# Kernel optimization log

Measured on AMD Instinct MI355X. Metric: run time of the kernel, lower is better.

## Reference

```python
import jax, jax.numpy as jnp
import numpy as np

SCALE = 1.0 / np.sqrt(128.0).astype(np.float32)  # 1/sqrt(head_dim)


def setup_inputs() -> dict:
    key = jax.random.key(0)
    kq, kk, kv = jax.random.split(key, 3)
    B, S, D = 32, 2048, 128
    q = jax.random.normal(kq, (B, S, D), dtype=jnp.float32)
    k = jax.random.normal(kk, (B, S, D), dtype=jnp.float32)
    v = jax.random.normal(kv, (B, S, D), dtype=jnp.float32)
    return {"q": q, "k": k, "v": v}


def reference(q, k, v):
    # attention = bmm(q, k^T) * scale ; softmax over last (key) dim; bmm with v
    scores = jnp.einsum("bsd,btd->bst", q, k) * SCALE  # [B, S, S]
    attn = jax.nn.softmax(scores, axis=-1)
    return jnp.einsum("bst,btd->bsd", attn, v)  # [B, S, D]
```

## Files before the change

### kernel.cpp

```cpp
#include <hip/hip_runtime.h>
#include <math.h>
#include <stdint.h>

typedef __bf16 bf16_t;
typedef __bf16 bf16x2 __attribute__((ext_vector_type(2)));
typedef __bf16 bf16x4 __attribute__((ext_vector_type(4)));
typedef __bf16 bf16x8 __attribute__((ext_vector_type(8)));
typedef float f32x4 __attribute__((ext_vector_type(4)));

#define NB   32
#define SEQ  2048
#define HD   128
#define SCALE 0.08838834764831845f
#define LOG2E 1.4426950408889634f

__device__ __forceinline__ float fast_exp2(float x) {
#if __has_builtin(__builtin_amdgcn_exp2f)
  return __builtin_amdgcn_exp2f(x);
#else
  return exp2f(x);
#endif
}

__global__ __launch_bounds__(256) void prep_kernel(
    const float* __restrict__ K, const float* __restrict__ V,
    bf16_t* __restrict__ Kb, bf16_t* __restrict__ Vt)
{
  const int b = blockIdx.x;
  const int tid = threadIdx.x;
  if (b < 2048) {
    size_t base4 = (size_t)b * 1024;
#pragma unroll
    for (int i = 0; i < 4; ++i) {
      size_t idx = base4 + tid + i * 256;
      float4 x = ((const float4*)K)[idx];
      bf16x4 y;
      y[0] = (bf16_t)x.x; y[1] = (bf16_t)x.y;
      y[2] = (bf16_t)x.z; y[3] = (bf16_t)x.w;
      ((bf16x4*)Kb)[idx] = y;
    }
  } else {
    __shared__ float tile[64][65];
    const int bt = b - 2048;
    const int batch = bt >> 6;
    const int rem = bt & 63;
    const int s0 = (rem >> 1) * 64;
    const int d0 = (rem & 1) * 64;
#pragma unroll
    for (int i = 0; i < 4; ++i) {
      int e = tid + i * 256;
      int s = e >> 4, dq = e & 15;
      float4 x = *(const float4*)&V[((size_t)batch * SEQ + s0 + s) * HD + d0 + dq * 4];
      tile[s][dq * 4 + 0] = x.x;
      tile[s][dq * 4 + 1] = x.y;
      tile[s][dq * 4 + 2] = x.z;
      tile[s][dq * 4 + 3] = x.w;
    }
    __syncthreads();
#pragma unroll
    for (int i = 0; i < 2; ++i) {
      int g = tid + i * 256;
      int d = g >> 3, sg = g & 7;
      bf16x8 w;
#pragma unroll
      for (int j = 0; j < 8; ++j) w[j] = (bf16_t)tile[sg * 8 + j][d];
      *(bf16x8*)&Vt[((size_t)batch * HD + d0 + d) * SEQ + s0 + sg * 8] = w;
    }
  }
}

__global__ __launch_bounds__(256) void fa6_kernel(
    const float* __restrict__ Q, const bf16_t* __restrict__ Kbf,
    const bf16_t* __restrict__ Vt, float* __restrict__ O)
{
  __shared__ __attribute__((aligned(16))) bf16_t Ksw[2][64 * 128];
  __shared__ __attribute__((aligned(16))) bf16_t Vsw[2][128 * 64];
  __shared__ __attribute__((aligned(16))) bf16_t Psh[4][16][72];

  const int tid  = threadIdx.x;
  const int lane = tid & 63;
  const int wq   = tid >> 6;
  const int quad = lane >> 4;
  const int l15  = lane & 15;

  const int batch = blockIdx.x >> 5;
  const int qt    = blockIdx.x & 31;

  const float*  Qb = Q   + ((size_t)batch * SEQ + qt * 64) * HD;
  const bf16_t* Kb = Kbf + (size_t)batch * SEQ * HD;
  const bf16_t* Vb = Vt  + (size_t)batch * HD * SEQ;
  float*        Ob = O   + ((size_t)batch * SEQ + qt * 64) * HD;

  bf16x8 aq[4];
  {
    const int qrow = wq * 16 + l15;
    const float qs = SCALE * LOG2E;
#pragma unroll
    for (int kf = 0; kf < 4; ++kf) {
      const float* qp = Qb + (size_t)qrow * HD + kf * 32 + quad * 8;
      float4 x0 = *(const float4*)qp;
      float4 x1 = *(const float4*)(qp + 4);
      bf16x8 a;
      a[0] = (bf16_t)(x0.x * qs); a[1] = (bf16_t)(x0.y * qs);
      a[2] = (bf16_t)(x0.z * qs); a[3] = (bf16_t)(x0.w * qs);
      a[4] = (bf16_t)(x1.x * qs); a[5] = (bf16_t)(x1.y * qs);
      a[6] = (bf16_t)(x1.z * qs); a[7] = (bf16_t)(x1.w * qs);
      aq[kf] = a;
    }
  }

  f32x4 o[8];
#pragma unroll
  for (int t = 0; t < 8; ++t) { o[t][0]=0.f; o[t][1]=0.f; o[t][2]=0.f; o[t][3]=0.f; }
  float m_r = -INFINITY, l_r = 0.0f;

  auto stage = [&](int buf, int kb) {
#pragma unroll
    for (int i = 0; i < 4; ++i) {
      int row = wq * 16 + i * 4 + (lane >> 4);
      int gk = (lane & 15) ^ (row & 15);
      const bf16_t* gp = Kb + (size_t)(kb + row) * HD + gk * 8;
      __builtin_amdgcn_global_load_lds(
          (const __attribute__((address_space(1))) void*)gp,
          (__attribute__((address_space(3))) void*)&Ksw[buf][(wq * 16 + i * 4) * 128],
          16, 0, 0);
    }
#pragma unroll
    for (int i = 0; i < 4; ++i) {
      int d = wq * 32 + i * 8 + (lane >> 3);
      int gv = (lane & 7) ^ (d & 7);
      const bf16_t* gp = Vb + (size_t)d * SEQ + kb + gv * 8;
      __builtin_amdgcn_global_load_lds(
          (const __attribute__((address_space(1))) void*)gp,
          (__attribute__((address_space(3))) void*)&Vsw[buf][(wq * 32 + i * 8) * 64],
          16, 0, 0);
    }
  };

  stage(0, 0);

  for (int it = 0; it < SEQ / 64; ++it) {
    __syncthreads();
    if (it + 1 < SEQ / 64) stage((it + 1) & 1, (it + 1) * 64);

    const bf16_t* Ks = &Ksw[it & 1][0];
    const bf16_t* Vs = &Vsw[it & 1][0];

    f32x4 s[4];
#pragma unroll
    for (int ct = 0; ct < 4; ++ct) { s[ct][0]=0.f; s[ct][1]=0.f; s[ct][2]=0.f; s[ct][3]=0.f; }
    __builtin_amdgcn_s_setprio(1);
#pragma unroll
    for (int kf = 0; kf < 4; ++kf)
#pragma unroll
      for (int ct = 0; ct < 4; ++ct) {
        int row = ct * 16 + l15;
        bf16x8 ak = *(const bf16x8*)&Ks[row * 128 + (((kf * 4 + quad) ^ l15) * 8)];
        s[ct] = __builtin_amdgcn_mfma_f32_16x16x32_bf16(ak, aq[kf], s[ct], 0, 0, 0);
      }
    __builtin_amdgcn_s_setprio(0);

    float mx = s[0][0];
#pragma unroll
    for (int ct = 0; ct < 4; ++ct)
#pragma unroll
      for (int r = 0; r < 4; ++r) mx = fmaxf(mx, s[ct][r]);
    mx = fmaxf(mx, __shfl_xor(mx, 16));
    mx = fmaxf(mx, __shfl_xor(mx, 32));

    bf16x8 av0[8], av1[8];
#pragma unroll
    for (int t = 0; t < 8; ++t) {
      const int d = t * 16 + l15;
      av0[t] = *(const bf16x8*)&Vs[d * 64 + ((quad ^ (l15 & 7)) * 8)];
      av1[t] = *(const bf16x8*)&Vs[d * 64 + (((4 + quad) ^ (l15 & 7)) * 8)];
    }

    if (!__all(mx <= m_r + 8.0f)) {
      const float mnew = fmaxf(m_r, mx);
      const float alpha = fast_exp2(m_r - mnew);
      m_r = mnew;
      l_r *= alpha;
#pragma unroll
      for (int t = 0; t < 8; ++t) {
        o[t][0]*=alpha; o[t][1]*=alpha; o[t][2]*=alpha; o[t][3]*=alpha;
      }
    }

    float ls = 0.f;
#pragma unroll
    for (int ct = 0; ct < 4; ++ct)
#pragma unroll
      for (int r = 0; r < 4; ++r) {
        float p = fast_exp2(s[ct][r] - m_r);
        s[ct][r] = p; ls += p;
      }

#pragma unroll
    for (int ct = 0; ct < 4; ++ct) {
      bf16x4 pp;
      pp[0]=(bf16_t)s[ct][0]; pp[1]=(bf16_t)s[ct][1];
      pp[2]=(bf16_t)s[ct][2]; pp[3]=(bf16_t)s[ct][3];
      *(bf16x4*)&Psh[wq][l15][ct * 16 + quad * 4] = pp;
    }
    ls += __shfl_xor(ls, 16);
    ls += __shfl_xor(ls, 32);
    l_r += ls;
    asm volatile("s_waitcnt lgkmcnt(0)" ::: "memory");
    bf16x8 ap0 = *(const bf16x8*)&Psh[wq][l15][quad * 8];
    bf16x8 ap1 = *(const bf16x8*)&Psh[wq][l15][32 + quad * 8];

    __builtin_amdgcn_s_setprio(1);
#pragma unroll
    for (int t = 0; t < 8; ++t) {
      o[t] = __builtin_amdgcn_mfma_f32_16x16x32_bf16(av0[t], ap0, o[t], 0, 0, 0);
      o[t] = __builtin_amdgcn_mfma_f32_16x16x32_bf16(av1[t], ap1, o[t], 0, 0, 0);
    }
    __builtin_amdgcn_s_setprio(0);
  }

  float inv = 1.0f / l_r;
  const int qrow = wq * 16 + l15;
#pragma unroll
  for (int t = 0; t < 8; ++t) {
    float4 w;
    w.x = o[t][0]*inv; w.y = o[t][1]*inv; w.z = o[t][2]*inv; w.w = o[t][3]*inv;
    *(float4*)&Ob[(size_t)qrow * HD + t * 16 + quad * 4] = w;
  }
}

#define BM   64
#define BN   64
#define KPAD 8
#define VPAD 8
#define PPAD 8

__global__ __launch_bounds__(256) void fa_fallback(
    const float* __restrict__ Q, const float* __restrict__ K,
    const float* __restrict__ V, float* __restrict__ O)
{
  __shared__ __attribute__((aligned(16))) bf16_t Ksh[BN][HD + KPAD];
  __shared__ __attribute__((aligned(16))) bf16_t Vsh[HD][BN + VPAD];
  __shared__ __attribute__((aligned(16))) bf16_t Psh[4][16][BN + PPAD];

  const int tid = threadIdx.x;
  const int lane = tid & 63;
  const int wq = tid >> 6;
  const int quad = lane >> 4;
  const int l15 = lane & 15;
  const int bid = blockIdx.x;
  const int batch = bid >> 5;
  const int qt = bid & 31;

  const float* Qb = Q + (size_t)batch * SEQ * HD + (size_t)qt * BM * HD;
  const float* Kb = K + (size_t)batch * SEQ * HD;
  const float* Vb = V + (size_t)batch * SEQ * HD;
  float* Ob = O + (size_t)batch * SEQ * HD + (size_t)qt * BM * HD;

  bf16x8 aq[4];
  {
    const int qrow = wq * 16 + l15;
#pragma unroll
    for (int kf = 0; kf < 4; ++kf) {
      const float* qp = Qb + (size_t)qrow * HD + kf * 32 + quad * 8;
      float4 x0 = *(const float4*)(qp);
      float4 x1 = *(const float4*)(qp + 4);
      bf16x8 a;
      a[0] = (bf16_t)(x0.x * SCALE); a[1] = (bf16_t)(x0.y * SCALE);
      a[2] = (bf16_t)(x0.z * SCALE); a[3] = (bf16_t)(x0.w * SCALE);
      a[4] = (bf16_t)(x1.x * SCALE); a[5] = (bf16_t)(x1.y * SCALE);
      a[6] = (bf16_t)(x1.z * SCALE); a[7] = (bf16_t)(x1.w * SCALE);
      aq[kf] = a;
    }
  }

  f32x4 o[8];
#pragma unroll
  for (int t = 0; t < 8; ++t) { o[t][0]=0.f; o[t][1]=0.f; o[t][2]=0.f; o[t][3]=0.f; }
  float m_r = -INFINITY, l_r = 0.0f;
  const int vkp = (tid & 31) * 2;
  const int vg = tid >> 5;
  float4 kreg[8], vreg[8];

#pragma unroll
  for (int i = 0; i < 8; ++i) {
    int v = tid + i * 256, row = v >> 5, c4 = (v & 31) * 4;
    kreg[i] = *(const float4*)(Kb + (size_t)row * HD + c4);
  }
#pragma unroll
  for (int i = 0; i < 4; ++i) {
    int d0 = (vg + i * 8) * 4;
    const float* vp0 = Vb + (size_t)vkp * HD + d0;
    vreg[2 * i] = *(const float4*)vp0;
    vreg[2 * i + 1] = *(const float4*)(vp0 + HD);
  }

  for (int kb = 0; kb < SEQ; kb += BN) {
    __syncthreads();
#pragma unroll
    for (int i = 0; i < 8; ++i) {
      int v = tid + i * 256, row = v >> 5, c4 = (v & 31) * 4;
      float4 kv = kreg[i];
      bf16x4 kk;
      kk[0]=(bf16_t)kv.x; kk[1]=(bf16_t)kv.y; kk[2]=(bf16_t)kv.z; kk[3]=(bf16_t)kv.w;
      *(bf16x4*)&Ksh[row][c4] = kk;
    }
#pragma unroll
    for (int i = 0; i < 4; ++i) {
      int d0 = (vg + i * 8) * 4;
      float4 a0 = vreg[2 * i], a1 = vreg[2 * i + 1];
      bf16x2 p0; p0[0]=(bf16_t)a0.x; p0[1]=(bf16_t)a1.x;
      bf16x2 p1; p1[0]=(bf16_t)a0.y; p1[1]=(bf16_t)a1.y;
      bf16x2 p2; p2[0]=(bf16_t)a0.z; p2[1]=(bf16_t)a1.z;
      bf16x2 p3; p3[0]=(bf16_t)a0.w; p3[1]=(bf16_t)a1.w;
      *(bf16x2*)&Vsh[d0 + 0][vkp] = p0;
      *(bf16x2*)&Vsh[d0 + 1][vkp] = p1;
      *(bf16x2*)&Vsh[d0 + 2][vkp] = p2;
      *(bf16x2*)&Vsh[d0 + 3][vkp] = p3;
    }
    __syncthreads();

    const int kbn = kb + BN;
    if (kbn < SEQ) {
#pragma unroll
      for (int i = 0; i < 8; ++i) {
        int v = tid + i * 256, row = v >> 5, c4 = (v & 31) * 4;
        kreg[i] = *(const float4*)(Kb + (size_t)(kbn + row) * HD + c4);
      }
#pragma unroll
      for (int i = 0; i < 4; ++i) {
        int d0 = (vg + i * 8) * 4;
        const float* vp0 = Vb + (size_t)(kbn + vkp) * HD + d0;
        vreg[2 * i] = *(const float4*)vp0;
        vreg[2 * i + 1] = *(const float4*)(vp0 + HD);
      }
    }

    f32x4 s[4];
#pragma unroll
    for (int ct = 0; ct < 4; ++ct) { s[ct][0]=0.f; s[ct][1]=0.f; s[ct][2]=0.f; s[ct][3]=0.f; }
#pragma unroll
    for (int kf = 0; kf < 4; ++kf)
#pragma unroll
      for (int ct = 0; ct < 4; ++ct) {
        bf16x8 ak = *(const bf16x8*)&Ksh[ct * 16 + l15][kf * 32 + quad * 8];
        s[ct] = __builtin_amdgcn_mfma_f32_16x16x32_bf16(ak, aq[kf], s[ct], 0, 0, 0);
      }

    float mx = s[0][0];
#pragma unroll
    for (int ct = 0; ct < 4; ++ct)
#pragma unroll
      for (int r = 0; r < 4; ++r) mx = fmaxf(mx, s[ct][r]);
    mx = fmaxf(mx, __shfl_xor(mx, 16));
    mx = fmaxf(mx, __shfl_xor(mx, 32));
    float mnew = fmaxf(m_r, mx);
    float alpha = __expf(m_r - mnew);
    m_r = mnew;
    float ls = 0.f;
#pragma unroll
    for (int ct = 0; ct < 4; ++ct)
#pragma unroll
      for (int r = 0; r < 4; ++r) {
        float p = __expf(s[ct][r] - mnew);
        s[ct][r] = p; ls += p;
      }
    ls += __shfl_xor(ls, 16);
    ls += __shfl_xor(ls, 32);
    l_r = l_r * alpha + ls;

#pragma unroll
    for (int ct = 0; ct < 4; ++ct) {
      bf16x4 pp;
      pp[0]=(bf16_t)s[ct][0]; pp[1]=(bf16_t)s[ct][1];
      pp[2]=(bf16_t)s[ct][2]; pp[3]=(bf16_t)s[ct][3];
      *(bf16x4*)&Psh[wq][l15][ct * 16 + quad * 4] = pp;
    }
    asm volatile("s_waitcnt lgkmcnt(0)" ::: "memory");
    bf16x8 ap0 = *(const bf16x8*)&Psh[wq][l15][quad * 8];
    bf16x8 ap1 = *(const bf16x8*)&Psh[wq][l15][32 + quad * 8];

#pragma unroll
    for (int t = 0; t < 8; ++t) {
      o[t][0]*=alpha; o[t][1]*=alpha; o[t][2]*=alpha; o[t][3]*=alpha;
    }
#pragma unroll
    for (int t = 0; t < 8; ++t) {
      bf16x8 av0 = *(const bf16x8*)&Vsh[t * 16 + l15][quad * 8];
      o[t] = __builtin_amdgcn_mfma_f32_16x16x32_bf16(av0, ap0, o[t], 0, 0, 0);
      bf16x8 av1 = *(const bf16x8*)&Vsh[t * 16 + l15][32 + quad * 8];
      o[t] = __builtin_amdgcn_mfma_f32_16x16x32_bf16(av1, ap1, o[t], 0, 0, 0);
    }
  }

  float inv = 1.0f / l_r;
  const int qrow = wq * 16 + l15;
#pragma unroll
  for (int t = 0; t < 8; ++t) {
    float4 w;
    w.x = o[t][0]*inv; w.y = o[t][1]*inv; w.z = o[t][2]*inv; w.w = o[t][3]*inv;
    *(float4*)&Ob[(size_t)qrow * HD + t * 16 + quad * 4] = w;
  }
}

extern "C" void kernel_launch(void* const* d_in, const int* in_sizes, int n_in,
                              void* d_out, int out_size, void* d_ws, size_t ws_size,
                              hipStream_t stream) {
  const float* q = (const float*)d_in[0];
  const float* k = (const float*)d_in[1];
  const float* v = (const float*)d_in[2];
  float* out = (float*)d_out;

  const size_t elems = (size_t)NB * SEQ * HD;
  const size_t need = elems * 2 * 2;

  if (ws_size >= need) {
    bf16_t* Kb = (bf16_t*)d_ws;
    bf16_t* Vt = Kb + elems;
    prep_kernel<<<4096, 256, 0, stream>>>(k, v, Kb, Vt);
    fa6_kernel<<<NB * (SEQ / 64), 256, 0, stream>>>(q, Kb, Vt, out);
  } else {
    fa_fallback<<<NB * (SEQ / BM), 256, 0, stream>>>(q, k, v, out);
  }
}
```

Measured before the change: 246.7 us.

## Process two 64-row query groups per block to reuse K/V tiles

```diff
diff --git a/kernel.cpp b/kernel.cpp
--- a/kernel.cpp
+++ b/kernel.cpp
@@ -69,7 +69,7 @@
   }
 }
 
-__global__ __launch_bounds__(256) void fa6_kernel(
+__global__ __launch_bounds__(256) void fa7_kernel(
     const float* __restrict__ Q, const bf16_t* __restrict__ Kbf,
     const bf16_t* __restrict__ Vt, float* __restrict__ O)
 {
@@ -83,36 +83,43 @@
   const int quad = lane >> 4;
   const int l15  = lane & 15;
 
-  const int batch = blockIdx.x >> 5;
-  const int qt    = blockIdx.x & 31;
-
-  const float*  Qb = Q   + ((size_t)batch * SEQ + qt * 64) * HD;
+  const int L     = ((blockIdx.x & 7) << 6) | (blockIdx.x >> 3);
+  const int batch = L >> 4;
+  const int qt    = L & 15;
+
+  const float*  Qb = Q   + ((size_t)batch * SEQ + qt * 128) * HD;
   const bf16_t* Kb = Kbf + (size_t)batch * SEQ * HD;
   const bf16_t* Vb = Vt  + (size_t)batch * HD * SEQ;
-  float*        Ob = O   + ((size_t)batch * SEQ + qt * 64) * HD;
-
-  bf16x8 aq[4];
+  float*        Ob = O   + ((size_t)batch * SEQ + qt * 128) * HD;
+
+  bf16x8 aq[2][4];
   {
-    const int qrow = wq * 16 + l15;
     const float qs = SCALE * LOG2E;
 #pragma unroll
-    for (int kf = 0; kf < 4; ++kf) {
-      const float* qp = Qb + (size_t)qrow * HD + kf * 32 + quad * 8;
-      float4 x0 = *(const float4*)qp;
-      float4 x1 = *(const float4*)(qp + 4);
-      bf16x8 a;
-      a[0] = (bf16_t)(x0.x * qs); a[1] = (bf16_t)(x0.y * qs);
-      a[2] = (bf16_t)(x0.z * qs); a[3] = (bf16_t)(x0.w * qs);
-      a[4] = (bf16_t)(x1.x * qs); a[5] = (bf16_t)(x1.y * qs);
-      a[6] = (bf16_t)(x1.z * qs); a[7] = (bf16_t)(x1.w * qs);
-      aq[kf] = a;
-    }
-  }
-
-  f32x4 o[8];
-#pragma unroll
-  for (int t = 0; t < 8; ++t) { o[t][0]=0.f; o[t][1]=0.f; o[t][2]=0.f; o[t][3]=0.f; }
-  float m_r = -INFINITY, l_r = 0.0f;
+    for (int g = 0; g < 2; ++g) {
+      const int qrow = g * 64 + wq * 16 + l15;
+#pragma unroll
+      for (int kf = 0; kf < 4; ++kf) {
+        const float* qp = Qb + (size_t)qrow * HD + kf * 32 + quad * 8;
+        float4 x0 = *(const float4*)qp;
+        float4 x1 = *(const float4*)(qp + 4);
+        bf16x8 a;
+        a[0] = (bf16_t)(x0.x * qs); a[1] = (bf16_t)(x0.y * qs);
+        a[2] = (bf16_t)(x0.z * qs); a[3] = (bf16_t)(x0.w * qs);
+        a[4] = (bf16_t)(x1.x * qs); a[5] = (bf16_t)(x1.y * qs);
+        a[6] = (bf16_t)(x1.z * qs); a[7] = (bf16_t)(x1.w * qs);
+        aq[g][kf] = a;
+      }
+    }
+  }
+
+  f32x4 o[2][8];
+#pragma unroll
+  for (int g = 0; g < 2; ++g)
+#pragma unroll
+    for (int t = 0; t < 8; ++t) { o[g][t][0]=0.f; o[g][t][1]=0.f; o[g][t][2]=0.f; o[g][t][3]=0.f; }
+  float m_r0 = -INFINITY, l_r0 = 0.0f;
+  float m_r1 = -INFINITY, l_r1 = 0.0f;
 
   auto stage = [&](int buf, int kb) {
 #pragma unroll
@@ -146,27 +153,77 @@
     const bf16_t* Ks = &Ksw[it & 1][0];
     const bf16_t* Vs = &Vsw[it & 1][0];
 
-    f32x4 s[4];
-#pragma unroll
-    for (int ct = 0; ct < 4; ++ct) { s[ct][0]=0.f; s[ct][1]=0.f; s[ct][2]=0.f; s[ct][3]=0.f; }
-    __builtin_amdgcn_s_setprio(1);
+    f32x4 s[2][4];
+#pragma unroll
+    for (int g = 0; g < 2; ++g)
+#pragma unroll
+      for (int ct = 0; ct < 4; ++ct) { s[g][ct][0]=0.f; s[g][ct][1]=0.f; s[g][ct][2]=0.f; s[g][ct][3]=0.f; }
 #pragma unroll
     for (int kf = 0; kf < 4; ++kf)
 #pragma unroll
       for (int ct = 0; ct < 4; ++ct) {
         int row = ct * 16 + l15;
         bf16x8 ak = *(const bf16x8*)&Ks[row * 128 + (((kf * 4 + quad) ^ l15) * 8)];
-        s[ct] = __builtin_amdgcn_mfma_f32_16x16x32_bf16(ak, aq[kf], s[ct], 0, 0, 0);
-      }
-    __builtin_amdgcn_s_setprio(0);
-
-    float mx = s[0][0];
+        s[0][ct] = __builtin_amdgcn_mfma_f32_16x16x32_bf16(ak, aq[0][kf], s[0][ct], 0, 0, 0);
+        s[1][ct] = __builtin_amdgcn_mfma_f32_16x16x32_bf16(ak, aq[1][kf], s[1][ct], 0, 0, 0);
+      }
+
+    float mx0 = s[0][0][0], mx1 = s[1][0][0];
 #pragma unroll
     for (int ct = 0; ct < 4; ++ct)
 #pragma unroll
-      for (int r = 0; r < 4; ++r) mx = fmaxf(mx, s[ct][r]);
-    mx = fmaxf(mx, __shfl_xor(mx, 16));
-    mx = fmaxf(mx, __shfl_xor(mx, 32));
+      for (int r = 0; r < 4; ++r) {
+        mx0 = fmaxf(mx0, s[0][ct][r]);
+        mx1 = fmaxf(mx1, s[1][ct][r]);
+      }
+    mx0 = fmaxf(mx0, __shfl_xor(mx0, 16));
+    mx1 = fmaxf(mx1, __shfl_xor(mx1, 16));
+    mx0 = fmaxf(mx0, __shfl_xor(mx0, 32));
+    mx1 = fmaxf(mx1, __shfl_xor(mx1, 32));
+
+    if (!__all(mx0 <= m_r0 + 8.0f)) {
+      const float mnew = fmaxf(m_r0, mx0);
+      const float alpha = fast_exp2(m_r0 - mnew);
+      m_r0 = mnew; l_r0 *= alpha;
+#pragma unroll
+      for (int t = 0; t < 8; ++t) {
+        o[0][t][0]*=alpha; o[0][t][1]*=alpha; o[0][t][2]*=alpha; o[0][t][3]*=alpha;
+      }
+    }
+    if (!__all(mx1 <= m_r1 + 8.0f)) {
+      const float mnew = fmaxf(m_r1, mx1);
+      const float alpha = fast_exp2(m_r1 - mnew);
+      m_r1 = mnew; l_r1 *= alpha;
+#pragma unroll
+      for (int t = 0; t < 8; ++t) {
+        o[1][t][0]*=alpha; o[1][t][1]*=alpha; o[1][t][2]*=alpha; o[1][t][3]*=alpha;
+      }
+    }
+
+    float ls0 = 0.f, ls1 = 0.f;
+#pragma unroll
+    for (int ct = 0; ct < 4; ++ct)
+#pragma unroll
+      for (int r = 0; r < 4; ++r) {
+        float p0 = fast_exp2(s[0][ct][r] - m_r0);
+        float p1 = fast_exp2(s[1][ct][r] - m_r1);
+        s[0][ct][r] = p0; ls0 += p0;
+        s[1][ct][r] = p1; ls1 += p1;
+      }
+
+#pragma unroll
+    for (int ct = 0; ct < 4; ++ct) {
+      bf16x4 pp;
+      pp[0]=(bf16_t)s[0][ct][0]; pp[1]=(bf16_t)s[0][ct][1];
+      pp[2]=(bf16_t)s[0][ct][2]; pp[3]=(bf16_t)s[0][ct][3];
+      *(bf16x4*)&Psh[wq][l15][ct * 16 + quad * 4] = pp;
+    }
+    ls0 += __shfl_xor(ls0, 16);
+    ls0 += __shfl_xor(ls0, 32);
+    l_r0 += ls0;
+    asm volatile("s_waitcnt lgkmcnt(0)" ::: "memory");
+    bf16x8 ap0 = *(const bf16x8*)&Psh[wq][l15][quad * 8];
+    bf16x8 ap1 = *(const bf16x8*)&Psh[wq][l15][32 + quad * 8];
 
     bf16x8 av0[8], av1[8];
 #pragma unroll
@@ -174,58 +231,46 @@
       const int d = t * 16 + l15;
       av0[t] = *(const bf16x8*)&Vs[d * 64 + ((quad ^ (l15 & 7)) * 8)];
       av1[t] = *(const bf16x8*)&Vs[d * 64 + (((4 + quad) ^ (l15 & 7)) * 8)];
-    }
-
-    if (!__all(mx <= m_r + 8.0f)) {
-      const float mnew = fmaxf(m_r, mx);
-      const float alpha = fast_exp2(m_r - mnew);
-      m_r = mnew;
-      l_r *= alpha;
-#pragma unroll
-      for (int t = 0; t < 8; ++t) {
-        o[t][0]*=alpha; o[t][1]*=alpha; o[t][2]*=alpha; o[t][3]*=alpha;
-      }
-    }
-
-    float ls = 0.f;
-#pragma unroll
-    for (int ct = 0; ct < 4; ++ct)
-#pragma unroll
-      for (int r = 0; r < 4; ++r) {
-        float p = fast_exp2(s[ct][r] - m_r);
-        s[ct][r] = p; ls += p;
-      }
+      o[0][t] = __builtin_amdgcn_mfma_f32_16x16x32_bf16(av0[t], ap0, o[0][t], 0, 0, 0);
+      o[0][t] = __builtin_amdgcn_mfma_f32_16x16x32_bf16(av1[t], ap1, o[0][t], 0, 0, 0);
+    }
 
 #pragma unroll
     for (int ct = 0; ct < 4; ++ct) {
       bf16x4 pp;
-      pp[0]=(bf16_t)s[ct][0]; pp[1]=(bf16_t)s[ct][1];
-      pp[2]=(bf16_t)s[ct][2]; pp[3]=(bf16_t)s[ct][3];
+      pp[0]=(bf16_t)s[1][ct][0]; pp[1]=(bf16_t)s[1][ct][1];
+      pp[2]=(bf16_t)s[1][ct][2]; pp[3]=(bf16_t)s[1][ct][3];
       *(bf16x4*)&Psh[wq][l15][ct * 16 + quad * 4] = pp;
     }
-    ls += __shfl_xor(ls, 16);
-    ls += __shfl_xor(ls, 32);
-    l_r += ls;
+    ls1 += __shfl_xor(ls1, 16);
+    ls1 += __shfl_xor(ls1, 32);
+    l_r1 += ls1;
     asm volatile("s_waitcnt lgkmcnt(0)" ::: "memory");
-    bf16x8 ap0 = *(const bf16x8*)&Psh[wq][l15][quad * 8];
-    bf16x8 ap1 = *(const bf16x8*)&Psh[wq][l15][32 + quad * 8];
-
-    __builtin_amdgcn_s_setprio(1);
+    bf16x8 bp0 = *(const bf16x8*)&Psh[wq][l15][quad * 8];
+    bf16x8 bp1 = *(const bf16x8*)&Psh[wq][l15][32 + quad * 8];
+
 #pragma unroll
     for (int t = 0; t < 8; ++t) {
-      o[t] = __builtin_amdgcn_mfma_f32_16x16x32_bf16(av0[t], ap0, o[t], 0, 0, 0);
-      o[t] = __builtin_amdgcn_mfma_f32_16x16x32_bf16(av1[t], ap1, o[t], 0, 0, 0);
-    }
-    __builtin_amdgcn_s_setprio(0);
-  }
-
-  float inv = 1.0f / l_r;
-  const int qrow = wq * 16 + l15;
-#pragma unroll
-  for (int t = 0; t < 8; ++t) {
-    float4 w;
-    w.x = o[t][0]*inv; w.y = o[t][1]*inv; w.z = o[t][2]*inv; w.w = o[t][3]*inv;
-    *(float4*)&Ob[(size_t)qrow * HD + t * 16 + quad * 4] = w;
+      o[1][t] = __builtin_amdgcn_mfma_f32_16x16x32_bf16(av0[t], bp0, o[1][t], 0, 0, 0);
+      o[1][t] = __builtin_amdgcn_mfma_f32_16x16x32_bf16(av1[t], bp1, o[1][t], 0, 0, 0);
+    }
+  }
+
+  {
+    float inv0 = 1.0f / l_r0;
+    float inv1 = 1.0f / l_r1;
+#pragma unroll
+    for (int g = 0; g < 2; ++g) {
+      const float inv = g ? inv1 : inv0;
+      const int qrow = g * 64 + wq * 16 + l15;
+#pragma unroll
+      for (int t = 0; t < 8; ++t) {
+        float4 w;
+        w.x = o[g][t][0]*inv; w.y = o[g][t][1]*inv;
+        w.z = o[g][t][2]*inv; w.w = o[g][t][3]*inv;
+        *(float4*)&Ob[(size_t)qrow * HD + t * 16 + quad * 4] = w;
+      }
+    }
   }
 }
 
@@ -418,7 +463,7 @@
     bf16_t* Kb = (bf16_t*)d_ws;
     bf16_t* Vt = Kb + elems;
     prep_kernel<<<4096, 256, 0, stream>>>(k, v, Kb, Vt);
-    fa6_kernel<<<NB * (SEQ / 64), 256, 0, stream>>>(q, Kb, Vt, out);
+    fa7_kernel<<<NB * (SEQ / 128), 256, 0, stream>>>(q, Kb, Vt, out);
   } else {
     fa_fallback<<<NB * (SEQ / BM), 256, 0, stream>>>(q, k, v, out);
   }
```

Measured after the change: 258.6 us. 4.8% more time.

## Load V fragments directly into registers with double buffering, bypassing LDS

Applied to the files above, without the earlier changes.

```diff
diff --git a/kernel.cpp b/kernel.cpp
--- a/kernel.cpp
+++ b/kernel.cpp
@@ -69,12 +69,11 @@
   }
 }
 
-__global__ __launch_bounds__(256) void fa6_kernel(
+__global__ __launch_bounds__(256) void fa11_kernel(
     const float* __restrict__ Q, const bf16_t* __restrict__ Kbf,
     const bf16_t* __restrict__ Vt, float* __restrict__ O)
 {
   __shared__ __attribute__((aligned(16))) bf16_t Ksw[2][64 * 128];
-  __shared__ __attribute__((aligned(16))) bf16_t Vsw[2][128 * 64];
   __shared__ __attribute__((aligned(16))) bf16_t Psh[4][16][72];
 
   const int tid  = threadIdx.x;
@@ -114,7 +113,7 @@
   for (int t = 0; t < 8; ++t) { o[t][0]=0.f; o[t][1]=0.f; o[t][2]=0.f; o[t][3]=0.f; }
   float m_r = -INFINITY, l_r = 0.0f;
 
-  auto stage = [&](int buf, int kb) {
+  auto stageK = [&](int buf, int kb) {
 #pragma unroll
     for (int i = 0; i < 4; ++i) {
       int row = wq * 16 + i * 4 + (lane >> 4);
@@ -125,31 +124,31 @@
           (__attribute__((address_space(3))) void*)&Ksw[buf][(wq * 16 + i * 4) * 128],
           16, 0, 0);
     }
-#pragma unroll
-    for (int i = 0; i < 4; ++i) {
-      int d = wq * 32 + i * 8 + (lane >> 3);
-      int gv = (lane & 7) ^ (d & 7);
-      const bf16_t* gp = Vb + (size_t)d * SEQ + kb + gv * 8;
-      __builtin_amdgcn_global_load_lds(
-          (const __attribute__((address_space(1))) void*)gp,
-          (__attribute__((address_space(3))) void*)&Vsw[buf][(wq * 32 + i * 8) * 64],
-          16, 0, 0);
-    }
   };
 
-  stage(0, 0);
-
-  for (int it = 0; it < SEQ / 64; ++it) {
+  bf16x8 avA[16], avB[16];
+
+  auto loadV = [&](bf16x8 (&av)[16], int kb) {
+#pragma unroll
+    for (int i = 0; i < 8; ++i) {
+      const bf16_t* vp = Vb + (size_t)(i * 16 + l15) * SEQ + kb;
+      av[i]     = *(const bf16x8*)&vp[quad * 8];
+      av[8 + i] = *(const bf16x8*)&vp[32 + quad * 8];
+    }
+  };
+
+  auto body = [&](int t, bf16x8 (&avc)[16], bf16x8 (&avn)[16]) {
     __syncthreads();
-    if (it + 1 < SEQ / 64) stage((it + 1) & 1, (it + 1) * 64);
-
-    const bf16_t* Ks = &Ksw[it & 1][0];
-    const bf16_t* Vs = &Vsw[it & 1][0];
+    if (t + 1 < SEQ / 64) {
+      stageK((t + 1) & 1, (t + 1) * 64);
+      loadV(avn, (t + 1) * 64);
+    }
+
+    const bf16_t* Ks = &Ksw[t & 1][0];
 
     f32x4 s[4];
 #pragma unroll
     for (int ct = 0; ct < 4; ++ct) { s[ct][0]=0.f; s[ct][1]=0.f; s[ct][2]=0.f; s[ct][3]=0.f; }
-    __builtin_amdgcn_s_setprio(1);
 #pragma unroll
     for (int kf = 0; kf < 4; ++kf)
 #pragma unroll
@@ -158,7 +157,6 @@
         bf16x8 ak = *(const bf16x8*)&Ks[row * 128 + (((kf * 4 + quad) ^ l15) * 8)];
         s[ct] = __builtin_amdgcn_mfma_f32_16x16x32_bf16(ak, aq[kf], s[ct], 0, 0, 0);
       }
-    __builtin_amdgcn_s_setprio(0);
 
     float mx = s[0][0];
 #pragma unroll
@@ -167,14 +165,6 @@
       for (int r = 0; r < 4; ++r) mx = fmaxf(mx, s[ct][r]);
     mx = fmaxf(mx, __shfl_xor(mx, 16));
     mx = fmaxf(mx, __shfl_xor(mx, 32));
-
-    bf16x8 av0[8], av1[8];
-#pragma unroll
-    for (int t = 0; t < 8; ++t) {
-      const int d = t * 16 + l15;
-      av0[t] = *(const bf16x8*)&Vs[d * 64 + ((quad ^ (l15 & 7)) * 8)];
-      av1[t] = *(const bf16x8*)&Vs[d * 64 + (((4 + quad) ^ (l15 & 7)) * 8)];
-    }
 
     if (!__all(mx <= m_r + 8.0f)) {
       const float mnew = fmaxf(m_r, mx);
@@ -182,8 +172,8 @@
       m_r = mnew;
       l_r *= alpha;
 #pragma unroll
-      for (int t = 0; t < 8; ++t) {
-        o[t][0]*=alpha; o[t][1]*=alpha; o[t][2]*=alpha; o[t][3]*=alpha;
+      for (int tt = 0; tt < 8; ++tt) {
+        o[tt][0]*=alpha; o[tt][1]*=alpha; o[tt][2]*=alpha; o[tt][3]*=alpha;
       }
     }
 
@@ -195,6 +185,9 @@
         float p = fast_exp2(s[ct][r] - m_r);
         s[ct][r] = p; ls += p;
       }
+    ls += __shfl_xor(ls, 16);
+    ls += __shfl_xor(ls, 32);
+    l_r += ls;
 
 #pragma unroll
     for (int ct = 0; ct < 4; ++ct) {
@@ -203,20 +196,23 @@
       pp[2]=(bf16_t)s[ct][2]; pp[3]=(bf16_t)s[ct][3];
       *(bf16x4*)&Psh[wq][l15][ct * 16 + quad * 4] = pp;
     }
-    ls += __shfl_xor(ls, 16);
-    ls += __shfl_xor(ls, 32);
-    l_r += ls;
     asm volatile("s_waitcnt lgkmcnt(0)" ::: "memory");
     bf16x8 ap0 = *(const bf16x8*)&Psh[wq][l15][quad * 8];
     bf16x8 ap1 = *(const bf16x8*)&Psh[wq][l15][32 + quad * 8];
 
-    __builtin_amdgcn_s_setprio(1);
-#pragma unroll
-    for (int t = 0; t < 8; ++t) {
-      o[t] = __builtin_amdgcn_mfma_f32_16x16x32_bf16(av0[t], ap0, o[t], 0, 0, 0);
-      o[t] = __builtin_amdgcn_mfma_f32_16x16x32_bf16(av1[t], ap1, o[t], 0, 0, 0);
-    }
-    __builtin_amdgcn_s_setprio(0);
+#pragma unroll
+    for (int tt = 0; tt < 8; ++tt) {
+      o[tt] = __builtin_amdgcn_mfma_f32_16x16x32_bf16(avc[tt],     ap0, o[tt], 0, 0, 0);
+      o[tt] = __builtin_amdgcn_mfma_f32_16x16x32_bf16(avc[8 + tt], ap1, o[tt], 0, 0, 0);
+    }
+  };
+
+  stageK(0, 0);
+  loadV(avA, 0);
+
+  for (int t = 0; t < SEQ / 64; t += 2) {
+    body(t,     avA, avB);
+    body(t + 1, avB, avA);
   }
 
   float inv = 1.0f / l_r;
@@ -418,7 +414,7 @@
     bf16_t* Kb = (bf16_t*)d_ws;
     bf16_t* Vt = Kb + elems;
     prep_kernel<<<4096, 256, 0, stream>>>(k, v, Kb, Vt);
-    fa6_kernel<<<NB * (SEQ / 64), 256, 0, stream>>>(q, Kb, Vt, out);
+    fa11_kernel<<<NB * (SEQ / 64), 256, 0, stream>>>(q, Kb, Vt, out);
   } else {
     fa_fallback<<<NB * (SEQ / BM), 256, 0, stream>>>(q, k, v, out);
   }
```

New measurement: 454.3 us. +84.1%, slower.
